# Kernel tuning notes

Measured on AMD Instinct MI355X. Metric: run time of the kernel, lower is better.

## Reference

```python
import jax, jax.numpy as jnp
import numpy as np

NUM_HEADS = 12


def setup_inputs() -> dict:
    key = jax.random.key(0)
    k1, k2, k3, k4, k5 = jax.random.split(key, 5)
    B, N, C = 4, 1024, 768
    x = jax.random.normal(k1, (B, N, C), dtype=jnp.float32)
    y = jax.random.normal(k2, (B, N, C), dtype=jnp.float32)
    w_qkv = jax.random.normal(k3, (4 * C, C), dtype=jnp.float32) * 0.02
    w_proj = jax.random.normal(k4, (C, C), dtype=jnp.float32) * 0.02
    b_proj = jax.random.normal(k5, (C,), dtype=jnp.float32) * 0.02
    return {"x": x, "y": y, "w_qkv": w_qkv, "w_proj": w_proj, "b_proj": b_proj}


def reference(x, y, w_qkv, w_proj, b_proj):
    B, N, C = x.shape
    H = NUM_HEADS
    hd = C // H
    scale = hd ** (-0.5)

    def qkv4(t):
        # Linear(dim, 4*dim, bias=False): t @ W^T -> [B,N,4C] -> [4,B,H,N,hd]
        p = (t @ w_qkv.T).reshape(B, N, 4, H, hd).transpose(2, 0, 3, 1, 4)
        return p[0], p[1], p[2], p[3]

    qxo, qx, kx, vx = qkv4(x)
    qyo, qy, ky, _vy_from_y = qkv4(y)
    vy = vx  # faithful to source: vy = qkv[3] (from x), not qkv2[3]

    def attend(q, k, v, neg):
        s = jnp.einsum('bhnd,bhmd->bhnm', q, k) * scale
        a = jax.nn.softmax(-s if neg else s, axis=-1)
        o = jnp.einsum('bhnm,bhmd->bhnd', a, v)
        return o.transpose(0, 2, 1, 3).reshape(B, N, C)

    x_self = attend(qx, kx, vx, False)
    y_self = attend(qy, ky, vy, False)
    x_cross = attend(qyo, kx, vx, True)   # attnx = -(qyo @ kx^T)
    y_cross = attend(qxo, ky, vy, True)   # attny = -(qxo @ ky^T)

    out_x = (x_self + x_cross) @ w_proj.T + b_proj
    out_y = (y_self + y_cross) @ w_proj.T + b_proj
    return (out_x, out_y)
```

## Files before the change

kernel.cpp:

```cpp
#include <hip/hip_runtime.h>
#include <hip/hip_bf16.h>
#include <stdint.h>


#define BB 4
#define NN 1024
#define CC 768
#define HH 12
#define HD 64

typedef unsigned short u16;
typedef short short8 __attribute__((ext_vector_type(8)));
typedef float f32x4 __attribute__((ext_vector_type(4)));

extern "C" __device__ float __ocml_native_exp2_f32(float);

__device__ __forceinline__ u16 f2bf(float f) {
  unsigned int u = __float_as_uint(f);
  return (u16)((u + 0x7fffu + ((u >> 16) & 1u)) >> 16);
}

__device__ __forceinline__ void load_lds16(const u16* g, u16* l) {
  __builtin_amdgcn_global_load_lds((__attribute__((address_space(1))) const void*)g,
                                   (__attribute__((address_space(3))) void*)l, 16, 0, 0);
}

__global__ __launch_bounds__(256)
void cvt_bf16(const float* __restrict__ x, const float* __restrict__ y,
              const float* __restrict__ wq, const float* __restrict__ wp,
              u16* __restrict__ xb, u16* __restrict__ yb,
              u16* __restrict__ wqb, u16* __restrict__ wpb)
{
  const int seg = blockIdx.y;
  const float* src = seg == 0 ? x : (seg == 1 ? y : (seg == 2 ? wq : wp));
  u16* dst = seg == 0 ? xb : (seg == 1 ? yb : (seg == 2 ? wqb : wpb));
  const int n = (seg == 3) ? 768 * 768 : ((seg == 2) ? 3072 * 768 : 4096 * 768);
  const int i = (blockIdx.x * 256 + threadIdx.x) * 8;
  if (i >= n) return;
  float sc = 1.0f;
  if (seg == 2) {
    const int row = i / 768;
    sc = (row < 768) ? -0.18033688f : (row < 1536 ? 0.18033688f : 1.0f);
  }
  float4 a = *(const float4*)(src + i);
  float4 b = *(const float4*)(src + i + 4);
  ushort4 u0 = {f2bf(a.x * sc), f2bf(a.y * sc), f2bf(a.z * sc), f2bf(a.w * sc)};
  ushort4 u1 = {f2bf(b.x * sc), f2bf(b.y * sc), f2bf(b.z * sc), f2bf(b.w * sc)};
  *(ushort4*)(dst + i) = u0;
  *(ushort4*)(dst + i + 4) = u1;
}

template<int NP, bool BF16OUT, bool BIAS, int NZ1, bool VSPLIT>
__global__ __launch_bounds__(512, 4)
void gemm_mfma(const u16* __restrict__ A0, const u16* __restrict__ A1,
               const u16* __restrict__ W, const float* __restrict__ bias,
               void* __restrict__ C0, void* __restrict__ C1,
               u16* __restrict__ VTout)
{
  __shared__ u16 As[128 * 64];
  __shared__ u16 Bs[128 * 64];
  const int m0 = blockIdx.y * 128, n0 = blockIdx.x * 128;
  if (blockIdx.z && n0 >= NZ1) return;
  const u16* A = blockIdx.z ? A1 : A0;
  void* C = blockIdx.z ? C1 : C0;
  const int t = threadIdx.x, w = t >> 6, lane = t & 63;
  const int c = lane & 15, qq = lane >> 4;
  const int mq = (w >> 2) * 64, nq = (w & 3) * 32;

  const int lr = lane >> 3;
  const int lchunk = (lane & 7) ^ lr;
  int arow[2], brow[2];
#pragma unroll
  for (int i = 0; i < 2; i++) {
    const int r = (w * 2 + i) * 8 + lr;
    arow[i] = (m0 + r) * 768 + lchunk * 8;
    brow[i] = (n0 + r) * 768 + lchunk * 8;
  }

  f32x4 acc[4][2] = {};
  for (int k0 = 0; k0 < 768; k0 += 64) {
    __syncthreads();
#pragma unroll
    for (int i = 0; i < 2; i++) {
      load_lds16(A + arow[i] + k0, As + (w * 2 + i) * 512);
      load_lds16(W + brow[i] + k0, Bs + (w * 2 + i) * 512);
    }
    __syncthreads();
#pragma unroll
    for (int s = 0; s < 2; s++) {
      const int swz = ((s * 4 + qq) ^ (c & 7)) * 8;
      short8 af[4], bf[2];
#pragma unroll
      for (int i = 0; i < 4; i++)
        af[i] = *(const short8*)&As[(mq + i * 16 + c) * 64 + swz];
#pragma unroll
      for (int j = 0; j < 2; j++)
        bf[j] = *(const short8*)&Bs[(nq + j * 16 + c) * 64 + swz];
#pragma unroll
      for (int i = 0; i < 4; i++)
#pragma unroll
        for (int j = 0; j < 2; j++)
          acc[i][j] = __builtin_amdgcn_mfma_f32_16x16x32_bf16(af[i], bf[j], acc[i][j], 0, 0, 0);
    }
  }

  if (VSPLIT && blockIdx.z == 0 && n0 >= 2304) {
#pragma unroll
    for (int i = 0; i < 4; i++)
#pragma unroll
      for (int r = 0; r < 4; r++) {
        const int m = m0 + mq + i * 16 + qq * 4 + r;
        const int b_ = m >> 10, key = m & 1023;
        const int kt = key >> 5, kk = key & 31;
        const int mcol = kt * 32 + ((kk >> 2) & 3) * 8 + ((kk >> 4) & 1) * 4 + (kk & 3);
#pragma unroll
        for (int j = 0; j < 2; j++) {
          const int pl = n0 - 2304 + nq + c + j * 16;
          const int h_ = pl >> 6, d_ = pl & 63;
          VTout[(size_t)((b_ * HH + h_) * 64 + d_) * 1024 + mcol] = f2bf(acc[i][j][r]);
        }
      }
    return;
  }

  float bj[2] = {0.f, 0.f};
  if (BIAS) {
#pragma unroll
    for (int j = 0; j < 2; j++) bj[j] = bias[n0 + nq + c + j * 16];
  }
#pragma unroll
  for (int i = 0; i < 4; i++)
#pragma unroll
    for (int r = 0; r < 4; r++) {
      const size_t row = (size_t)(m0 + mq + i * 16 + qq * 4 + r) * NP + n0 + nq + c;
      if (BF16OUT) {
#pragma unroll
        for (int j = 0; j < 2; j++)
          ((u16*)C)[row + j * 16] = f2bf(acc[i][j][r]);
      } else {
#pragma unroll
        for (int j = 0; j < 2; j++)
          ((float*)C)[row + j * 16] = acc[i][j][r] + bj[j];
      }
    }
}

__global__ __launch_bounds__(256, 4)
void attn_pair_mfma(const u16* __restrict__ qkvx, const u16* __restrict__ qkvy,
                    const u16* __restrict__ VT,
                    u16* __restrict__ sum_x, u16* __restrict__ sum_y)
{
  __shared__ __align__(16) u16 smem[18432];
  float (*Of)[68] = (float(*)[68])smem;

  const int blk = blockIdx.x;
  const int xcd = blk & 7, slot = blk >> 3;
  const int bh = (slot >> 5) * 8 + xcd;
  const int inner = slot & 31;
  const int qt = inner >> 1, pair = inner & 1;
  const int b = bh / HH, head = bh % HH;
  const u16* q1 = pair ? qkvy : qkvx;
  const u16* q2 = pair ? qkvx : qkvy;
  const u16* ks = pair ? qkvy : qkvx;
  u16* outp = pair ? sum_y : sum_x;

  const int t = threadIdx.x, w = t >> 6, lane = t & 63;
  const int c = lane & 15, qq = lane >> 4;

  short8 Qf[2][2];
  {
    const int qrow = qt * 64 + w * 16 + c;
    const u16* qs = q1 + (size_t)(b * NN + qrow) * 3072 + CC + head * HD + qq * 8;
    const u16* qc = q2 + (size_t)(b * NN + qrow) * 3072 + head * HD + qq * 8;
    Qf[0][0] = *(const short8*)qs;
    Qf[0][1] = *(const short8*)(qs + 32);
    Qf[1][0] = *(const short8*)qc;
    Qf[1][1] = *(const short8*)(qc + 32);
  }

  const u16* kbase = ks + (size_t)(b * NN) * 3072 + 2 * CC + head * HD;
  const u16* vtb = VT + (size_t)(bh * 64) * 1024;

  const int lr = lane >> 3;
  const int sc8 = ((lane & 7) ^ lr) * 8;

  short8 ones;
#pragma unroll
  for (int i = 0; i < 8; i++) ones[i] = (short)0x3F80;

  f32x4 O[2][4] = {};
  f32x4 L[2] = {};

  const int cx = c & 7;
  const int koff0 = (qq ^ cx) * 8;
  const int koff1 = ((4 + qq) ^ cx) * 8;

#pragma unroll
  for (int i = 0; i < 2; i++) {
    const int r = (2 * w + i) * 8 + lr;
    load_lds16(kbase + (size_t)r * 3072 + sc8, smem + (2 * w + i) * 512);
    load_lds16(vtb + (size_t)r * 1024 + sc8, smem + 8192 + (2 * w + i) * 512);
  }
  __syncthreads();

  for (int c16 = 0; c16 < 16; ++c16) {
    const int cur = c16 & 1;
    const u16* Kb = smem + cur * 4096;
    const u16* Vb = smem + 8192 + cur * 4096;

    if (c16 < 15) {
      u16* Kn = smem + (cur ^ 1) * 4096;
      u16* Vn = smem + 8192 + (cur ^ 1) * 4096;
#pragma unroll
      for (int i = 0; i < 2; i++) {
        const int r = (2 * w + i) * 8 + lr;
        load_lds16(kbase + (size_t)((c16 + 1) * 64 + r) * 3072 + sc8,
                   Kn + (2 * w + i) * 512);
        load_lds16(vtb + (size_t)r * 1024 + (c16 + 1) * 64 + sc8,
                   Vn + (2 * w + i) * 512);
      }
    }

    __builtin_amdgcn_s_setprio(1);

    unsigned pk[2][4][2];
#pragma unroll
    for (int t4 = 0; t4 < 4; t4++) {
      const u16* kr = Kb + (16 * t4 + c) * 64;
      short8 k0 = *(const short8*)(kr + koff0);
      short8 k1 = *(const short8*)(kr + koff1);
#pragma unroll
      for (int s = 0; s < 2; s++) {
        f32x4 z = {0.f, 0.f, 0.f, 0.f};
        z = __builtin_amdgcn_mfma_f32_16x16x32_bf16(k0, Qf[s][0], z, 0, 0, 0);
        z = __builtin_amdgcn_mfma_f32_16x16x32_bf16(k1, Qf[s][1], z, 0, 0, 0);
        unsigned int u0 = __float_as_uint(__ocml_native_exp2_f32(z[0]));
        unsigned int u1 = __float_as_uint(__ocml_native_exp2_f32(z[1]));
        unsigned int u2 = __float_as_uint(__ocml_native_exp2_f32(z[2]));
        unsigned int u3 = __float_as_uint(__ocml_native_exp2_f32(z[3]));
        pk[s][t4][0] = __builtin_amdgcn_perm(u1, u0, 0x07060302u);
        pk[s][t4][1] = __builtin_amdgcn_perm(u3, u2, 0x07060302u);
      }
    }

    short8 pa[2][2];
#pragma unroll
    for (int s = 0; s < 2; s++) {
      union { unsigned u[4]; short8 s8; } f0, f1;
      f0.u[0] = pk[s][0][0]; f0.u[1] = pk[s][0][1];
      f0.u[2] = pk[s][1][0]; f0.u[3] = pk[s][1][1];
      f1.u[0] = pk[s][2][0]; f1.u[1] = pk[s][2][1];
      f1.u[2] = pk[s][3][0]; f1.u[3] = pk[s][3][1];
      pa[s][0] = f0.s8;
      pa[s][1] = f1.s8;
      L[s] = __builtin_amdgcn_mfma_f32_16x16x32_bf16(pa[s][0], ones, L[s], 0, 0, 0);
      L[s] = __builtin_amdgcn_mfma_f32_16x16x32_bf16(pa[s][1], ones, L[s], 0, 0, 0);
    }

#pragma unroll
    for (int t4 = 0; t4 < 4; t4++) {
      const u16* vr = Vb + (16 * t4 + c) * 64;
      short8 v0 = *(const short8*)(vr + koff0);
      short8 v1 = *(const short8*)(vr + koff1);
#pragma unroll
      for (int s = 0; s < 2; s++) {
        O[s][t4] = __builtin_amdgcn_mfma_f32_16x16x32_bf16(pa[s][0], v0, O[s][t4], 0, 0, 0);
        O[s][t4] = __builtin_amdgcn_mfma_f32_16x16x32_bf16(pa[s][1], v1, O[s][t4], 0, 0, 0);
      }
    }

    __builtin_amdgcn_s_setprio(0);

    __syncthreads();
  }

  float is[4], ic[4];
#pragma unroll
  for (int r = 0; r < 4; r++) {
    is[r] = 1.0f / L[0][r];
    ic[r] = 1.0f / L[1][r];
  }
#pragma unroll
  for (int t4 = 0; t4 < 4; t4++)
#pragma unroll
    for (int r = 0; r < 4; r++)
      Of[w * 16 + 4 * qq + r][16 * t4 + c] =
          O[0][t4][r] * is[r] + O[1][t4][r] * ic[r];
  __syncthreads();
#pragma unroll
  for (int p = 0; p < 4; p++) {
    const int idx = p * 256 + t;
    const int row = idx >> 4, c4 = (idx & 15) * 4;
    float4 v = *(const float4*)&Of[row][c4];
    ushort4 u = {f2bf(v.x), f2bf(v.y), f2bf(v.z), f2bf(v.w)};
    *(ushort4*)(outp + (size_t)(b * NN + qt * 64 + row) * CC + head * HD + c4) = u;
  }
}

extern "C" void kernel_launch(void* const* d_in, const int* in_sizes, int n_in,
                              void* d_out, int out_size, void* d_ws, size_t ws_size,
                              hipStream_t stream)
{
  const float* x      = (const float*)d_in[0];
  const float* y      = (const float*)d_in[1];
  const float* w_qkv  = (const float*)d_in[2];
  const float* w_proj = (const float*)d_in[3];
  const float* b_proj = (const float*)d_in[4];

  u16* qkv_x = (u16*)d_ws;
  u16* qkv_y = qkv_x + (size_t)4096 * 3072;
  u16* rest = qkv_y + (size_t)4096 * 3072;
  u16* sum_x = rest;
  u16* sum_y = sum_x + (size_t)4096 * 768;
  u16* x_bf  = rest;
  u16* y_bf  = x_bf + (size_t)4096 * 768;
  u16* wq_bf = y_bf + (size_t)4096 * 768;
  u16* wp_bf = wq_bf + (size_t)3072 * 768;
  u16* VT    = wp_bf + (size_t)768 * 768;
  float* out_x = (float*)d_out;
  float* out_y = out_x + (size_t)4096 * 768;

  cvt_bf16<<<dim3(1536, 4), 256, 0, stream>>>(x, y, w_qkv, w_proj,
                                              x_bf, y_bf, wq_bf, wp_bf);

  gemm_mfma<3072, true, false, 2304, true><<<dim3(24, 32, 2), 512, 0, stream>>>(
      x_bf, y_bf, wq_bf, nullptr, qkv_x, qkv_y, VT);

  attn_pair_mfma<<<dim3(1536), 256, 0, stream>>>(qkv_x, qkv_y, VT, sum_x, sum_y);

  gemm_mfma<768, false, true, 768, false><<<dim3(6, 32, 2), 512, 0, stream>>>(
      sum_x, sum_y, wp_bf, b_proj, out_x, out_y, nullptr);
}
```

Measured before the change: 200.6 us.

## Double-buffer GEMM LDS tiles and remap QKV GEMM blocks per XCD

The GEMM kernel now keeps two LDS buffers and issues the global-to-LDS loads for the next K tile while MFMAs run on the current one. This cuts the loop to one barrier per step instead of two and overlaps memory latency with compute. The QKV GEMM also switches to a 1D grid with an XCD-aware mapping, so blocks on the same XCD share A and W tiles in L2. LDS use doubles to 64KB per block, which may lower occupancy below the launch-bounds target.

```diff
diff --git a/kernel.cpp b/kernel.cpp
--- a/kernel.cpp
+++ b/kernel.cpp
@@ -50,19 +50,37 @@
   *(ushort4*)(dst + i + 4) = u1;
 }
 
-template<int NP, bool BF16OUT, bool BIAS, int NZ1, bool VSPLIT>
+template<int NP, bool BF16OUT, bool BIAS, int NZ1, bool VSPLIT, bool SWZ>
 __global__ __launch_bounds__(512, 4)
 void gemm_mfma(const u16* __restrict__ A0, const u16* __restrict__ A1,
                const u16* __restrict__ W, const float* __restrict__ bias,
                void* __restrict__ C0, void* __restrict__ C1,
                u16* __restrict__ VTout)
 {
-  __shared__ u16 As[128 * 64];
-  __shared__ u16 Bs[128 * 64];
-  const int m0 = blockIdx.y * 128, n0 = blockIdx.x * 128;
-  if (blockIdx.z && n0 >= NZ1) return;
-  const u16* A = blockIdx.z ? A1 : A0;
-  void* C = blockIdx.z ? C1 : C0;
+  __shared__ u16 As[2][128 * 64];
+  __shared__ u16 Bs[2][128 * 64];
+
+  int m_t, n_t, z_;
+  if (SWZ) {
+    const int id = blockIdx.x;
+    z_ = blockIdx.y;
+    if (z_ == 0) {
+      const int xcd = id & 7, slot = id >> 3;
+      m_t = (xcd >> 2) * 16 + (slot & 15);
+      n_t = (xcd & 3) * 6 + (slot >> 4);
+    } else {
+      if (id >= 576) return;
+      const int xcd = id & 7, slot = id >> 3;
+      m_t = (xcd >> 1) * 8 + (slot & 7);
+      n_t = (xcd & 1) * 9 + (slot >> 3);
+    }
+  } else {
+    m_t = blockIdx.y; n_t = blockIdx.x; z_ = blockIdx.z;
+  }
+  const int m0 = m_t * 128, n0 = n_t * 128;
+  if (!SWZ && z_ && n0 >= NZ1) return;
+  const u16* A = z_ ? A1 : A0;
+  void* C = z_ ? C1 : C0;
   const int t = threadIdx.x, w = t >> 6, lane = t & 63;
   const int c = lane & 15, qq = lane >> 4;
   const int mq = (w >> 2) * 64, nq = (w & 3) * 32;
@@ -77,34 +95,44 @@
     brow[i] = (n0 + r) * 768 + lchunk * 8;
   }
 
+#pragma unroll
+  for (int i = 0; i < 2; i++) {
+    load_lds16(A + arow[i], As[0] + (w * 2 + i) * 512);
+    load_lds16(W + brow[i], Bs[0] + (w * 2 + i) * 512);
+  }
+  __syncthreads();
+
   f32x4 acc[4][2] = {};
-  for (int k0 = 0; k0 < 768; k0 += 64) {
-    __syncthreads();
-#pragma unroll
-    for (int i = 0; i < 2; i++) {
-      load_lds16(A + arow[i] + k0, As + (w * 2 + i) * 512);
-      load_lds16(W + brow[i] + k0, Bs + (w * 2 + i) * 512);
-    }
-    __syncthreads();
+  for (int kt = 0; kt < 12; ++kt) {
+    const int cur = kt & 1;
+    if (kt < 11) {
+      const int k1 = (kt + 1) * 64;
+#pragma unroll
+      for (int i = 0; i < 2; i++) {
+        load_lds16(A + arow[i] + k1, As[cur ^ 1] + (w * 2 + i) * 512);
+        load_lds16(W + brow[i] + k1, Bs[cur ^ 1] + (w * 2 + i) * 512);
+      }
+    }
 #pragma unroll
     for (int s = 0; s < 2; s++) {
       const int swz = ((s * 4 + qq) ^ (c & 7)) * 8;
       short8 af[4], bf[2];
 #pragma unroll
       for (int i = 0; i < 4; i++)
-        af[i] = *(const short8*)&As[(mq + i * 16 + c) * 64 + swz];
+        af[i] = *(const short8*)&As[cur][(mq + i * 16 + c) * 64 + swz];
 #pragma unroll
       for (int j = 0; j < 2; j++)
-        bf[j] = *(const short8*)&Bs[(nq + j * 16 + c) * 64 + swz];
+        bf[j] = *(const short8*)&Bs[cur][(nq + j * 16 + c) * 64 + swz];
 #pragma unroll
       for (int i = 0; i < 4; i++)
 #pragma unroll
         for (int j = 0; j < 2; j++)
           acc[i][j] = __builtin_amdgcn_mfma_f32_16x16x32_bf16(af[i], bf[j], acc[i][j], 0, 0, 0);
     }
-  }
-
-  if (VSPLIT && blockIdx.z == 0 && n0 >= 2304) {
+    __syncthreads();
+  }
+
+  if (VSPLIT && z_ == 0 && n0 >= 2304) {
 #pragma unroll
     for (int i = 0; i < 4; i++)
 #pragma unroll
@@ -323,11 +351,11 @@
   cvt_bf16<<<dim3(1536, 4), 256, 0, stream>>>(x, y, w_qkv, w_proj,
                                               x_bf, y_bf, wq_bf, wp_bf);
 
-  gemm_mfma<3072, true, false, 2304, true><<<dim3(24, 32, 2), 512, 0, stream>>>(
+  gemm_mfma<3072, true, false, 2304, true, true><<<dim3(768, 2), 512, 0, stream>>>(
       x_bf, y_bf, wq_bf, nullptr, qkv_x, qkv_y, VT);
 
   attn_pair_mfma<<<dim3(1536), 256, 0, stream>>>(qkv_x, qkv_y, VT, sum_x, sum_y);
 
-  gemm_mfma<768, false, true, 768, false><<<dim3(6, 32, 2), 512, 0, stream>>>(
+  gemm_mfma<768, false, true, 768, false, false><<<dim3(6, 32, 2), 512, 0, stream>>>(
       sum_x, sum_y, wp_bf, b_proj, out_x, out_y, nullptr);
 }
```

Measured after the change: 212.1 us. +5.8%, slower.
